# Optimization experiments

Measured on AMD Instinct MI355X. Metric: run time of the kernel, lower is better.

## Reference

```python
import jax, jax.numpy as jnp
import numpy as np

OBS_LEN = 8
N_PED = 2048      # total pedestrians
G = 64            # number of scenes (uniform size)
NP = N_PED // G   # pedestrians per scene = 32
H = 128           # action_decoder_hidden_dim == action_encoder_hidden_dim == f_in == f_out
DIN = 64          # action_encoder_input_dim
DD = 64           # distance_embedding_dim
NH = 4            # n_heads (hard-coded to 4 in GAT)


def setup_inputs() -> dict:
    key = jax.random.key(0)
    ks = jax.random.split(key, 16)
    s = 0.1  # weight scale (xavier-ish)
    starts = (jnp.arange(G) * NP).astype(jnp.int64)
    seq_start_end = jnp.stack([starts, starts + NP], axis=1)
    return {
        "obs_traj": jax.random.normal(ks[0], (OBS_LEN, N_PED, 2), jnp.float32),
        "goal_hidden_state": jax.random.normal(ks[1], (N_PED, H), jnp.float32),
        "goal": jax.random.normal(ks[2], (N_PED, 2), jnp.float32),
        "action": jax.random.normal(ks[3], (N_PED, 2), jnp.float32),
        "h0": jax.random.normal(ks[4], (N_PED, H), jnp.float32),
        "c0": jax.random.normal(ks[5], (N_PED, H), jnp.float32),
        "W_emb": jax.random.normal(ks[6], (2, DIN), jnp.float32) * s,
        "b_emb": jnp.zeros((DIN,), jnp.float32),
        "W_ih": jax.random.normal(ks[7], (4 * H, DIN), jnp.float32) * s,
        "W_hh": jax.random.normal(ks[8], (4 * H, H), jnp.float32) * s,
        "b_ih": jnp.zeros((4 * H,), jnp.float32),
        "b_hh": jnp.zeros((4 * H,), jnp.float32),
        "W_dist": jax.random.normal(ks[9], (8, DD), jnp.float32) * s,
        "b_dist": jnp.zeros((DD,), jnp.float32),
        "W_gate": jax.random.normal(ks[10], (DD, H), jnp.float32) * s,
        "b_gate": jnp.zeros((H,), jnp.float32),
        "gat_w": jax.random.normal(ks[11], (NH, 1, H, H), jnp.float32) * s,
        "gat_a": jax.random.normal(ks[12], (1, 1, 2 * H, 1), jnp.float32) * s,
        "gat_bias": jnp.zeros((H,), jnp.float32),
        "seq_start_end": seq_start_end,
    }


def _forward(obs_traj, goal_hidden_state, goal, action, h0, c0,
             W_emb, b_emb, W_ih, W_hh, b_ih, b_hh,
             W_dist, b_dist, W_gate, b_gate, gat_w, gat_a, gat_bias,
             seq_start_end):
    T, N, _ = obs_traj.shape
    g_num = seq_start_end.shape[0]
    n = N // g_num  # uniform group size

    # --- ActionEncoder: embed + LSTMCell loop over obs_len (lax.scan) ---
    x = jax.nn.relu(obs_traj.reshape(-1, 2) @ W_emb + b_emb).reshape(T, N, -1)

    def lstm_step(carry, xt):
        h, c = carry
        gates = xt @ W_ih.T + b_ih + h @ W_hh.T + b_hh  # torch gate order i,f,g,o
        i, f, g, o = jnp.split(gates, 4, axis=-1)
        c = jax.nn.sigmoid(f) * c + jax.nn.sigmoid(i) * jnp.tanh(g)
        h = jax.nn.sigmoid(o) * jnp.tanh(c)
        return (h, c), None

    (action_hidden, _), _ = jax.lax.scan(lstm_step, (h0, c0), x)  # [N, H]

    Hd = action_hidden.shape[-1]
    ahg = action_hidden.reshape(g_num, n, Hd)
    ghg = goal_hidden_state.reshape(g_num, n, Hd)
    glg = goal.reshape(g_num, n, 2)
    acg = action.reshape(g_num, n, 2)

    eye = jnp.eye(n, dtype=action_hidden.dtype)[:, :, None]  # [n, n, 1]

    def gat_group(ah, gh, gl, ac):
        # InteractionGate.cal_gate: dist[i,j] = [action_i, goal_i, action_j, goal_j]
        a_i = jnp.broadcast_to(ac[:, None, :], (n, n, 2))
        g_i = jnp.broadcast_to(gl[:, None, :], (n, n, 2))
        a_j = jnp.broadcast_to(ac[None, :, :], (n, n, 2))
        g_j = jnp.broadcast_to(gl[None, :, :], (n, n, 2))
        dist = jnp.concatenate([a_i, g_i, a_j, g_j], axis=-1)  # [n, n, 8]
        gate = jax.nn.sigmoid(jax.nn.relu(dist @ W_dist + b_dist) @ W_gate + b_gate)  # [n, n, H]

        # gate_action[i,j] = gate[i,j] * tanh(action_hidden[j])
        gate_action = gate * jnp.tanh(ah[None, :, :])
        # diagonal -> goal_hidden[i], off-diag -> gated action
        goal_action = eye * gh[None, :, :] + (1.0 - eye) * gate_action  # [n, n, H]

        h_other = jnp.concatenate([ah[:, None, :], goal_action], axis=1)  # [n, n+1, H]
        h_self = jnp.broadcast_to(ah[:, None, :], (n, n + 1, Hd))          # [n, n+1, H]

        # GraphAttentionLayer
        w = gat_w[:, 0]  # [NH, H, H]
        hs = jnp.einsum('nkf,hfo->hnko', h_self, w)   # [NH, n, n+1, H]
        ho = jnp.einsum('nkf,hfo->hnko', h_other, w)  # [NH, n, n+1, H]
        scores = jnp.concatenate([hs, ho], axis=-1) @ gat_a[0, 0, :, 0]  # [NH, n, n+1]
        alpha = jax.nn.softmax(jax.nn.leaky_relu(scores, 0.2), axis=-1)
        out = jnp.mean(jnp.sum(alpha[..., None] * ho, axis=2), axis=0)  # [n, H]
        return jax.nn.relu(out) + gat_bias

    out = jax.vmap(gat_group)(ahg, ghg, glg, acg)  # [G, n, H]
    return out.reshape(N, Hd)


def reference(obs_traj, goal_hidden_state, goal, action, h0, c0,
              W_emb, b_emb, W_ih, W_hh, b_ih, b_hh,
              W_dist, b_dist, W_gate, b_gate, gat_w, gat_a, gat_bias,
              seq_start_end):
    return _forward(obs_traj, goal_hidden_state, goal, action, h0, c0,
                    W_emb, b_emb, W_ih, W_hh, b_ih, b_hh,
                    W_dist, b_dist, W_gate, b_gate, gat_w, gat_a, gat_bias,
                    seq_start_end)
```

## Files before the change

kernel.cpp:

```cpp
#include <hip/hip_runtime.h>

#define N_PED 2048
#define NGROUP 64
#define NPG 32
#define HDIM 128
#define DIN 64
#define DDIM 64
#define NHEAD 4
#define TOBS 8

typedef __attribute__((ext_vector_type(8))) short bf16x8;
typedef __attribute__((ext_vector_type(4))) float f32x4;

__device__ __forceinline__ float sigm(float x){
    return __builtin_amdgcn_rcpf(1.f + __expf(-x));
}
__device__ __forceinline__ float tanh_fast(float x){
    return 1.f - 2.f*__builtin_amdgcn_rcpf(__expf(2.f*x) + 1.f);
}
__device__ __forceinline__ short f2bf(float f){
    unsigned u = __float_as_uint(f);
    unsigned r = (u + 0x7fffu + ((u >> 16) & 1u)) >> 16;
    return (short)r;
}
__device__ __forceinline__ float bf2f(unsigned short b){
    return __uint_as_float(((unsigned)b) << 16);
}
__device__ __forceinline__ unsigned pk2(float a, float b){
    return (unsigned)(unsigned short)f2bf(a) | ((unsigned)(unsigned short)f2bf(b) << 16);
}

#define WS_AHB   0
#define WS_TAHB  524288
#define WS_VW    1048576
#define WS_GF    1052672
#define WS_WF    1069056

__global__ __launch_bounds__(512) void prep_pack_kernel(
    const float* __restrict__ gat_w, const float* __restrict__ gat_a,
    const float* __restrict__ W_gate, unsigned char* __restrict__ ws)
{
    const int tid = threadIdx.x;
    if (blockIdx.x < 16) {
        __shared__ float sa[2*HDIM];
        __shared__ float red[32][8][2];
        float* VW = (float*)(ws + WS_VW);
        if (tid < 256) sa[tid] = gat_a[tid];
        __syncthreads();
        const int rl = (tid & 255) >> 3, ch = tid & 7;
        const int row = blockIdx.x*32 + rl;
        if (tid < 256) {
            const float* rp = gat_w + (size_t)row*HDIM + ch*16;
            float v = 0.f, w1 = 0.f;
            #pragma unroll
            for (int e = 0; e < 16; ++e) {
                float wv = rp[e];
                v  += wv * sa[HDIM + ch*16 + e];
                w1 += wv * sa[ch*16 + e];
            }
            red[rl][ch][0] = v; red[rl][ch][1] = w1;
        }
        __syncthreads();
        if (tid < 256 && ch == 0) {
            float sv = 0.f, sw = 0.f;
            #pragma unroll
            for (int e = 0; e < 8; ++e) { sv += red[rl][e][0]; sw += red[rl][e][1]; }
            VW[row]       = sv;
            VW[512 + row] = sw;
        }
    } else {
        const int id = (blockIdx.x - 16)*512 + tid;
        if (id >= 9216) return;
        uint4* Gf4 = reinterpret_cast<uint4*>(ws + WS_GF);
        uint4* Wf4 = reinterpret_cast<uint4*>(ws + WS_WF);
        if (id < 1024) {
            const int fid = id >> 6, L = id & 63;
            const int kt = fid >> 3, nt = fid & 7;
            const int q = L >> 4, ln = L & 15;
            float v[8];
            #pragma unroll
            for (int j = 0; j < 8; ++j)
                v[j] = W_gate[(size_t)(kt*32 + q*8 + j)*HDIM + nt*16 + ln];
            Gf4[id] = uint4{ pk2(v[0],v[1]), pk2(v[2],v[3]), pk2(v[4],v[5]), pk2(v[6],v[7]) };
        } else {
            const int id2 = id - 1024;
            const int fid = id2 >> 6, L = id2 & 63;
            const int kt = fid >> 3, nt = fid & 7;
            const int q = L >> 4, ln = L & 15;
            float v[8];
            #pragma unroll
            for (int j = 0; j < 8; ++j) {
                int F = kt*32 + q*8 + j;
                v[j] = gat_w[(size_t)(F >> 7)*16384 + (size_t)(F & 127)*HDIM + nt*16 + ln];
            }
            Wf4[id2] = uint4{ pk2(v[0],v[1]), pk2(v[2],v[3]), pk2(v[4],v[5]), pk2(v[6],v[7]) };
        }
    }
}

#define KPAD 216
__global__ __launch_bounds__(512, 1) void lstm_kernel(
    const float* __restrict__ obs, const float* __restrict__ h0,
    const float* __restrict__ c0,  const float* __restrict__ W_emb,
    const float* __restrict__ b_emb, const float* __restrict__ W_ih,
    const float* __restrict__ W_hh,  const float* __restrict__ b_ih,
    const float* __restrict__ b_hh,
    unsigned short* __restrict__ AHb, unsigned short* __restrict__ TAHb)
{
    __shared__ short Xl[2][16][KPAD];
    __shared__ float sEmb[192];

    const int tid  = threadIdx.x;
    const int ped0 = blockIdx.x * 8;
    const int w    = tid >> 6;
    const int lane = tid & 63;
    const int q    = lane >> 4;
    const int ln   = lane & 15;
    const int u    = w*16 + ln;

    if (tid < 192) sEmb[tid] = (tid < 128) ? W_emb[tid] : b_emb[tid - 128];

    bf16x8 bfr[4][6];
    #pragma unroll
    for (int idx = 0; idx < 4; ++idx) {
        const int n = idx*128 + u;
        #pragma unroll
        for (int kt = 0; kt < 6; ++kt) {
            const float* src = (kt < 2) ? (W_ih + (size_t)n*DIN  + kt*32 + q*8)
                                        : (W_hh + (size_t)n*HDIM + (kt-2)*32 + q*8);
            bf16x8 b;
            #pragma unroll
            for (int j = 0; j < 8; ++j) b[j] = f2bf(src[j]);
            bfr[idx][kt] = b;
        }
    }
    float bsv[4];
    #pragma unroll
    for (int idx = 0; idx < 4; ++idx) bsv[idx] = b_ih[idx*128 + u] + b_hh[idx*128 + u];

    float c_st[4];
    #pragma unroll
    for (int reg = 0; reg < 4; ++reg)
        c_st[reg] = c0[(size_t)(ped0 + ((q*4 + reg) & 7))*HDIM + u];

    #pragma unroll
    for (int reg = 0; reg < 4; ++reg)
        Xl[0][q*4 + reg][64 + u] = f2bf(h0[(size_t)(ped0 + ((q*4 + reg) & 7))*HDIM + u]);
    {
        const int pr = tid >> 5, d0 = (tid & 31)*2;
        const float2 ob = reinterpret_cast<const float2*>(obs)[(size_t)(ped0 + (pr & 7))];
        float x0 = fmaxf(ob.x*sEmb[d0]   + ob.y*sEmb[64+d0]   + sEmb[128+d0],   0.f);
        float x1 = fmaxf(ob.x*sEmb[d0+1] + ob.y*sEmb[64+d0+1] + sEmb[128+d0+1], 0.f);
        *reinterpret_cast<unsigned*>(&Xl[0][pr][d0]) = pk2(x0, x1);
    }
    __syncthreads();

    float hval[4];
    #pragma unroll
    for (int t = 0; t < TOBS; ++t) {
        const int cur = t & 1, nxt = cur ^ 1;

        if (t < TOBS-1) {
            const int pr = tid >> 5, d0 = (tid & 31)*2;
            const float2 ob = reinterpret_cast<const float2*>(obs)[(size_t)((t+1)*N_PED + ped0 + (pr & 7))];
            float x0 = fmaxf(ob.x*sEmb[d0]   + ob.y*sEmb[64+d0]   + sEmb[128+d0],   0.f);
            float x1 = fmaxf(ob.x*sEmb[d0+1] + ob.y*sEmb[64+d0+1] + sEmb[128+d0+1], 0.f);
            *reinterpret_cast<unsigned*>(&Xl[nxt][pr][d0]) = pk2(x0, x1);
        }

        bf16x8 afr[6];
        #pragma unroll
        for (int kt = 0; kt < 6; ++kt)
            afr[kt] = *reinterpret_cast<const bf16x8*>(&Xl[cur][ln][kt*32 + q*8]);

        f32x4 acc[4];
        #pragma unroll
        for (int idx = 0; idx < 4; ++idx) {
            f32x4 a = { bsv[idx], bsv[idx], bsv[idx], bsv[idx] };
            #pragma unroll
            for (int kt = 0; kt < 6; ++kt)
                a = __builtin_amdgcn_mfma_f32_16x16x32_bf16(afr[kt], bfr[idx][kt], a, 0, 0, 0);
            acc[idx] = a;
        }
        #pragma unroll
        for (int reg = 0; reg < 4; ++reg) {
            float c = sigm(acc[1][reg])*c_st[reg] + sigm(acc[0][reg])*tanh_fast(acc[2][reg]);
            c_st[reg] = c;
            hval[reg] = sigm(acc[3][reg])*tanh_fast(c);
        }

        if (t < TOBS-1) {
            #pragma unroll
            for (int reg = 0; reg < 4; ++reg)
                Xl[nxt][q*4 + reg][64 + u] = f2bf(hval[reg]);
            __syncthreads();
        }
    }

    if (q < 2) {
        #pragma unroll
        for (int reg = 0; reg < 4; ++reg) {
            const size_t off = (size_t)(ped0 + q*4 + reg)*HDIM + u;
            AHb[off]  = (unsigned short)f2bf(hval[reg]);
            TAHb[off] = (unsigned short)f2bf(tanh_fast(hval[reg]));
        }
    }
}

__global__ __launch_bounds__(256) void gat_kernel(
    const unsigned short* __restrict__ AHb,
    const unsigned short* __restrict__ TAHb,
    const float* __restrict__ VW,
    const unsigned char* __restrict__ ws,
    const float* __restrict__ ghs,
    const float* __restrict__ goal,
    const float* __restrict__ action,
    const float* __restrict__ W_dist,
    const float* __restrict__ b_dist,
    const float* __restrict__ b_gate,
    const float* __restrict__ gat_bias,
    float* __restrict__ out)
{
    __shared__ unsigned short sGAb[80][136];
    __shared__ unsigned short sTAHb[32][136];
    __shared__ unsigned short st1b[64][72];
    __shared__ unsigned short sU[4][520];
    __shared__ float sAl[2][4][34];
    __shared__ float sPj[80][8];
    __shared__ float sWd[8][64];
    __shared__ float sbd[64];
    __shared__ float sbg[128];
    __shared__ float sgb[128];
    __shared__ float sAC[32][2], sGL[32][2];

    const int tid = threadIdx.x;
    const int g   = blockIdx.x >> 3;
    const int i0  = (blockIdx.x & 7) * 4;
    const int p0  = g * NPG;
    const int w   = tid >> 6;
    const int L   = tid & 63;
    const int q   = L >> 4;
    const int ln  = L & 15;

    const bf16x8* Gf8 = reinterpret_cast<const bf16x8*>(ws + WS_GF);
    const bf16x8* Wf8 = reinterpret_cast<const bf16x8*>(ws + WS_WF);

    for (int s = tid; s < 512; s += 256) {
        int j = s >> 4, c = s & 15;
        *reinterpret_cast<uint4*>(&sTAHb[j][c*8]) =
            *reinterpret_cast<const uint4*>(&TAHb[(size_t)(p0 + j)*HDIM + c*8]);
    }
    if (tid < 128) {
        sbg[tid] = b_gate[tid];
        sgb[tid] = gat_bias[tid];
    } else if (tid < 192) {
        sbd[tid-128] = b_dist[tid-128];
    } else {
        int j = tid - 192;
        int pd = j & 31;
        if (j < 32) { const float2 a = reinterpret_cast<const float2*>(action)[p0+pd];
                      sAC[pd][0]=a.x; sAC[pd][1]=a.y; }
        else        { const float2 gl = reinterpret_cast<const float2*>(goal)[p0+pd];
                      sGL[pd][0]=gl.x; sGL[pd][1]=gl.y; }
    }
    if (tid < 256) {
        int rr = tid >> 6, k = tid & 63;
        sWd[rr][k]   = W_dist[rr*64 + k];
        sWd[rr+4][k] = W_dist[(rr+4)*64 + k];
    }

    bf16x8 vf[4];
    #pragma unroll
    for (int kt = 0; kt < 4; ++kt) {
        bf16x8 b;
        #pragma unroll
        for (int j = 0; j < 8; ++j) {
            int k = kt*32 + q*8 + j;
            float v = 0.f;
            if (ln < 4)      v = VW[ln*HDIM + k];
            else if (ln < 8) v = VW[512 + (ln-4)*HDIM + k];
            b[j] = f2bf(v);
        }
        vf[kt] = b;
    }
    __syncthreads();

    for (int half = 0; half < 2; ++half) {
        {
            const int k = tid & 63, mg = tid >> 6;
            float base[2];
            #pragma unroll
            for (int rh = 0; rh < 2; ++rh) {
                int i = i0 + half*2 + rh;
                base[rh] = sAC[i][0]*sWd[0][k] + sAC[i][1]*sWd[1][k]
                         + sGL[i][0]*sWd[2][k] + sGL[i][1]*sWd[3][k] + sbd[k];
            }
            #pragma unroll
            for (int mm = 0; mm < 16; ++mm) {
                int m = mg*16 + mm, j = m & 31;
                float v = base[m>>5] + sAC[j][0]*sWd[4][k] + sAC[j][1]*sWd[5][k]
                                     + sGL[j][0]*sWd[6][k] + sGL[j][1]*sWd[7][k];
                st1b[m][k] = (unsigned short)f2bf(fmaxf(v, 0.f));
            }
        }
        __syncthreads();

        {
            bf16x8 afr[2];
            #pragma unroll
            for (int kt = 0; kt < 2; ++kt)
                afr[kt] = *reinterpret_cast<const bf16x8*>(&st1b[w*16 + ln][kt*32 + q*8]);
            for (int nt = 0; nt < 8; ++nt) {
                float bg = sbg[nt*16 + ln];
                f32x4 a = { bg, bg, bg, bg };
                a = __builtin_amdgcn_mfma_f32_16x16x32_bf16(afr[0], Gf8[(0*8+nt)*64 + L], a, 0, 0, 0);
                a = __builtin_amdgcn_mfma_f32_16x16x32_bf16(afr[1], Gf8[(1*8+nt)*64 + L], a, 0, 0, 0);
                #pragma unroll
                for (int reg = 0; reg < 4; ++reg) {
                    int mrow = w*16 + q*4 + reg;
                    int n = nt*16 + ln;
                    float ga = sigm(a[reg]) * bf2f(sTAHb[mrow & 31][n]);
                    sGAb[mrow][n] = (unsigned short)f2bf(ga);
                }
            }
        }
        __syncthreads();

        {
            int rh = tid >> 7, f = tid & 127;
            int irow = i0 + half*2 + rh;
            sGAb[rh*32 + irow][f] = (unsigned short)f2bf(ghs[(size_t)(p0 + irow)*HDIM + f]);
            sGAb[64 + rh][f]      = AHb[(size_t)(p0 + irow)*HDIM + f];
        }
        __syncthreads();

        {
            int nmt = (w == 0) ? 2 : 1;
            for (int e = 0; e < nmt; ++e) {
                int mt = (e == 0) ? w : 4;
                bf16x8 afr;
                f32x4 a = { 0.f, 0.f, 0.f, 0.f };
                #pragma unroll
                for (int kt = 0; kt < 4; ++kt) {
                    afr = *reinterpret_cast<const bf16x8*>(&sGAb[mt*16 + ln][kt*32 + q*8]);
                    a = __builtin_amdgcn_mfma_f32_16x16x32_bf16(afr, vf[kt], a, 0, 0, 0);
                }
                if (ln < 8) {
                    #pragma unroll
                    for (int reg = 0; reg < 4; ++reg)
                        sPj[mt*16 + q*4 + reg][ln] = a[reg];
                }
            }
        }
        __syncthreads();

        if (tid < 8) {
            int rh = tid >> 2, h = tid & 3;
            float sa_ = sPj[64 + rh][4 + h];
            float x0  = sa_ + sPj[64 + rh][h];
            x0 = (x0 < 0.f) ? 0.2f*x0 : x0;
            float sum = 1.f;
            sAl[rh][h][0] = 1.f;
            for (int k = 1; k <= 32; ++k) {
                float x = sa_ + sPj[rh*32 + k - 1][h];
                x = (x < 0.f) ? 0.2f*x : x;
                float e = __expf(x - x0);
                sAl[rh][h][k] = e; sum += e;
            }
            float inv = 1.f/sum;
            for (int k = 0; k <= 32; ++k) sAl[rh][h][k] *= inv;
        }
        __syncthreads();

        {
            int rh = w & 1, ntb = (w >> 1) * 4;
            int r  = half*2 + rh;
            bf16x8 afr;
            #pragma unroll
            for (int jj = 0; jj < 8; ++jj)
                afr[jj] = f2bf(sAl[rh][ln & 3][1 + q*8 + jj]);
            for (int t = 0; t < 4; ++t) {
                int nt = ntb + t;
                bf16x8 bfr;
                #pragma unroll
                for (int jj = 0; jj < 8; ++jj)
                    bfr[jj] = (short)sGAb[rh*32 + q*8 + jj][nt*16 + ln];
                f32x4 a = { 0.f, 0.f, 0.f, 0.f };
                a = __builtin_amdgcn_mfma_f32_16x16x32_bf16(afr, bfr, a, 0, 0, 0);
                if (L < 16) {
                    #pragma unroll
                    for (int reg = 0; reg < 4; ++reg) {
                        float uv = a[reg] + sAl[rh][reg][0] * bf2f(sGAb[64 + rh][nt*16 + ln]);
                        sU[r][reg*HDIM + nt*16 + ln] = (unsigned short)f2bf(uv);
                    }
                }
            }
        }
        __syncthreads();
    }

    {
        bf16x8 afr[16];
        #pragma unroll
        for (int kt = 0; kt < 16; ++kt)
            afr[kt] = *reinterpret_cast<const bf16x8*>(&sU[ln & 3][kt*32 + q*8]);
        for (int e = 0; e < 2; ++e) {
            int nt = w*2 + e;
            f32x4 a = { 0.f, 0.f, 0.f, 0.f };
            #pragma unroll
            for (int kt = 0; kt < 16; ++kt)
                a = __builtin_amdgcn_mfma_f32_16x16x32_bf16(afr[kt], Wf8[(kt*8+nt)*64 + L], a, 0, 0, 0);
            if (L < 16) {
                int o = nt*16 + ln;
                #pragma unroll
                for (int reg = 0; reg < 4; ++reg) {
                    float val = fmaxf(a[reg]*0.25f, 0.f) + sgb[o];
                    out[(size_t)(p0 + i0 + reg)*HDIM + o] = val;
                }
            }
        }
    }
}

extern "C" void kernel_launch(void* const* d_in, const int* in_sizes, int n_in,
                              void* d_out, int out_size, void* d_ws, size_t ws_size,
                              hipStream_t stream) {
    const float* obs      = (const float*)d_in[0];
    const float* ghs      = (const float*)d_in[1];
    const float* goal     = (const float*)d_in[2];
    const float* action   = (const float*)d_in[3];
    const float* h0       = (const float*)d_in[4];
    const float* c0       = (const float*)d_in[5];
    const float* W_emb    = (const float*)d_in[6];
    const float* b_emb    = (const float*)d_in[7];
    const float* W_ih     = (const float*)d_in[8];
    const float* W_hh     = (const float*)d_in[9];
    const float* b_ih     = (const float*)d_in[10];
    const float* b_hh     = (const float*)d_in[11];
    const float* W_dist   = (const float*)d_in[12];
    const float* b_dist   = (const float*)d_in[13];
    const float* W_gate   = (const float*)d_in[14];
    const float* b_gate   = (const float*)d_in[15];
    const float* gat_w    = (const float*)d_in[16];
    const float* gat_a    = (const float*)d_in[17];
    const float* gat_bias = (const float*)d_in[18];

    unsigned char* ws = (unsigned char*)d_ws;
    unsigned short* AHb  = (unsigned short*)(ws + WS_AHB);
    unsigned short* TAHb = (unsigned short*)(ws + WS_TAHB);
    float* VW            = (float*)(ws + WS_VW);
    float* out = (float*)d_out;

    hipLaunchKernelGGL(prep_pack_kernel, dim3(34), dim3(512), 0, stream,
                       gat_w, gat_a, W_gate, ws);
    hipLaunchKernelGGL(lstm_kernel, dim3(256), dim3(512), 0, stream,
                       obs, h0, c0, W_emb, b_emb, W_ih, W_hh, b_ih, b_hh, AHb, TAHb);
    hipLaunchKernelGGL(gat_kernel,  dim3(512), dim3(256), 0, stream,
                       AHb, TAHb, VW, ws, ghs, goal, action,
                       W_dist, b_dist, b_gate, gat_bias, out);
}
```

Baseline: 142.7 us.

## Merge prep into LSTM launch and split GAT work across twice as many blocks

Folds the weight-packing prep kernel into the LSTM kernel as extra blocks, which removes one kernel launch and lets the prep run alongside the LSTM. The GAT kernel now handles two query rows per block instead of looping over two halves of four, doubling the grid to 1024 blocks for more parallelism. In exchange, the per-scene gate MLP and projection work is recomputed by twice as many blocks. It also drops the unroll on the LSTM time loop, relaxes its launch bounds, and splits the softmax sum into four accumulators with a fast reciprocal.

```diff
diff --git a/kernel.cpp b/kernel.cpp
--- a/kernel.cpp
+++ b/kernel.cpp
@@ -36,81 +36,83 @@
 #define WS_GF    1052672
 #define WS_WF    1069056
 
-__global__ __launch_bounds__(512) void prep_pack_kernel(
-    const float* __restrict__ gat_w, const float* __restrict__ gat_a,
-    const float* __restrict__ W_gate, unsigned char* __restrict__ ws)
-{
-    const int tid = threadIdx.x;
-    if (blockIdx.x < 16) {
-        __shared__ float sa[2*HDIM];
-        __shared__ float red[32][8][2];
-        float* VW = (float*)(ws + WS_VW);
-        if (tid < 256) sa[tid] = gat_a[tid];
-        __syncthreads();
-        const int rl = (tid & 255) >> 3, ch = tid & 7;
-        const int row = blockIdx.x*32 + rl;
-        if (tid < 256) {
-            const float* rp = gat_w + (size_t)row*HDIM + ch*16;
-            float v = 0.f, w1 = 0.f;
-            #pragma unroll
-            for (int e = 0; e < 16; ++e) {
-                float wv = rp[e];
-                v  += wv * sa[HDIM + ch*16 + e];
-                w1 += wv * sa[ch*16 + e];
-            }
-            red[rl][ch][0] = v; red[rl][ch][1] = w1;
-        }
-        __syncthreads();
-        if (tid < 256 && ch == 0) {
-            float sv = 0.f, sw = 0.f;
-            #pragma unroll
-            for (int e = 0; e < 8; ++e) { sv += red[rl][e][0]; sw += red[rl][e][1]; }
-            VW[row]       = sv;
-            VW[512 + row] = sw;
-        }
-    } else {
-        const int id = (blockIdx.x - 16)*512 + tid;
-        if (id >= 9216) return;
-        uint4* Gf4 = reinterpret_cast<uint4*>(ws + WS_GF);
-        uint4* Wf4 = reinterpret_cast<uint4*>(ws + WS_WF);
-        if (id < 1024) {
-            const int fid = id >> 6, L = id & 63;
-            const int kt = fid >> 3, nt = fid & 7;
-            const int q = L >> 4, ln = L & 15;
-            float v[8];
-            #pragma unroll
-            for (int j = 0; j < 8; ++j)
-                v[j] = W_gate[(size_t)(kt*32 + q*8 + j)*HDIM + nt*16 + ln];
-            Gf4[id] = uint4{ pk2(v[0],v[1]), pk2(v[2],v[3]), pk2(v[4],v[5]), pk2(v[6],v[7]) };
-        } else {
-            const int id2 = id - 1024;
-            const int fid = id2 >> 6, L = id2 & 63;
-            const int kt = fid >> 3, nt = fid & 7;
-            const int q = L >> 4, ln = L & 15;
-            float v[8];
-            #pragma unroll
-            for (int j = 0; j < 8; ++j) {
-                int F = kt*32 + q*8 + j;
-                v[j] = gat_w[(size_t)(F >> 7)*16384 + (size_t)(F & 127)*HDIM + nt*16 + ln];
-            }
-            Wf4[id2] = uint4{ pk2(v[0],v[1]), pk2(v[2],v[3]), pk2(v[4],v[5]), pk2(v[6],v[7]) };
-        }
-    }
-}
-
 #define KPAD 216
-__global__ __launch_bounds__(512, 1) void lstm_kernel(
+__global__ __launch_bounds__(512) void lstm_prep_kernel(
     const float* __restrict__ obs, const float* __restrict__ h0,
     const float* __restrict__ c0,  const float* __restrict__ W_emb,
     const float* __restrict__ b_emb, const float* __restrict__ W_ih,
     const float* __restrict__ W_hh,  const float* __restrict__ b_ih,
     const float* __restrict__ b_hh,
+    const float* __restrict__ gat_w, const float* __restrict__ gat_a,
+    const float* __restrict__ W_gate,
+    unsigned char* __restrict__ ws,
     unsigned short* __restrict__ AHb, unsigned short* __restrict__ TAHb)
 {
+    const int tid = threadIdx.x;
+
+    if (blockIdx.x >= 256) {
+        const int vb = blockIdx.x - 256;
+        if (vb < 16) {
+            __shared__ float sa[2*HDIM];
+            __shared__ float red[32][8][2];
+            float* VW = (float*)(ws + WS_VW);
+            if (tid < 256) sa[tid] = gat_a[tid];
+            __syncthreads();
+            const int rl = (tid & 255) >> 3, ch = tid & 7;
+            const int row = vb*32 + rl;
+            if (tid < 256) {
+                const float* rp = gat_w + (size_t)row*HDIM + ch*16;
+                float v = 0.f, w1 = 0.f;
+                #pragma unroll
+                for (int e = 0; e < 16; ++e) {
+                    float wv = rp[e];
+                    v  += wv * sa[HDIM + ch*16 + e];
+                    w1 += wv * sa[ch*16 + e];
+                }
+                red[rl][ch][0] = v; red[rl][ch][1] = w1;
+            }
+            __syncthreads();
+            if (tid < 256 && ch == 0) {
+                float sv = 0.f, sw = 0.f;
+                #pragma unroll
+                for (int e = 0; e < 8; ++e) { sv += red[rl][e][0]; sw += red[rl][e][1]; }
+                VW[row]       = sv;
+                VW[512 + row] = sw;
+            }
+        } else {
+            const int id = (vb - 16)*512 + tid;
+            if (id >= 9216) return;
+            uint4* Gf4 = reinterpret_cast<uint4*>(ws + WS_GF);
+            uint4* Wf4 = reinterpret_cast<uint4*>(ws + WS_WF);
+            if (id < 1024) {
+                const int fid = id >> 6, L = id & 63;
+                const int kt = fid >> 3, nt = fid & 7;
+                const int q = L >> 4, ln = L & 15;
+                float v[8];
+                #pragma unroll
+                for (int j = 0; j < 8; ++j)
+                    v[j] = W_gate[(size_t)(kt*32 + q*8 + j)*HDIM + nt*16 + ln];
+                Gf4[id] = uint4{ pk2(v[0],v[1]), pk2(v[2],v[3]), pk2(v[4],v[5]), pk2(v[6],v[7]) };
+            } else {
+                const int id2 = id - 1024;
+                const int fid = id2 >> 6, L = id2 & 63;
+                const int kt = fid >> 3, nt = fid & 7;
+                const int q = L >> 4, ln = L & 15;
+                float v[8];
+                #pragma unroll
+                for (int j = 0; j < 8; ++j) {
+                    int F = kt*32 + q*8 + j;
+                    v[j] = gat_w[(size_t)(F >> 7)*16384 + (size_t)(F & 127)*HDIM + nt*16 + ln];
+                }
+                Wf4[id2] = uint4{ pk2(v[0],v[1]), pk2(v[2],v[3]), pk2(v[4],v[5]), pk2(v[6],v[7]) };
+            }
+        }
+        return;
+    }
+
     __shared__ short Xl[2][16][KPAD];
     __shared__ float sEmb[192];
 
-    const int tid  = threadIdx.x;
     const int ped0 = blockIdx.x * 8;
     const int w    = tid >> 6;
     const int lane = tid & 63;
@@ -156,7 +158,6 @@
     __syncthreads();
 
     float hval[4];
-    #pragma unroll
     for (int t = 0; t < TOBS; ++t) {
         const int cur = t & 1, nxt = cur ^ 1;
 
@@ -224,7 +225,7 @@
     __shared__ unsigned short sGAb[80][136];
     __shared__ unsigned short sTAHb[32][136];
     __shared__ unsigned short st1b[64][72];
-    __shared__ unsigned short sU[4][520];
+    __shared__ unsigned short sU[2][520];
     __shared__ float sAl[2][4][34];
     __shared__ float sPj[80][8];
     __shared__ float sWd[8][64];
@@ -234,8 +235,8 @@
     __shared__ float sAC[32][2], sGL[32][2];
 
     const int tid = threadIdx.x;
-    const int g   = blockIdx.x >> 3;
-    const int i0  = (blockIdx.x & 7) * 4;
+    const int g   = blockIdx.x >> 4;
+    const int i0  = (blockIdx.x & 15) * 2;
     const int p0  = g * NPG;
     const int w   = tid >> 6;
     const int L   = tid & 63;
@@ -285,125 +286,130 @@
     }
     __syncthreads();
 
-    for (int half = 0; half < 2; ++half) {
-        {
-            const int k = tid & 63, mg = tid >> 6;
-            float base[2];
-            #pragma unroll
-            for (int rh = 0; rh < 2; ++rh) {
-                int i = i0 + half*2 + rh;
-                base[rh] = sAC[i][0]*sWd[0][k] + sAC[i][1]*sWd[1][k]
-                         + sGL[i][0]*sWd[2][k] + sGL[i][1]*sWd[3][k] + sbd[k];
-            }
-            #pragma unroll
-            for (int mm = 0; mm < 16; ++mm) {
-                int m = mg*16 + mm, j = m & 31;
-                float v = base[m>>5] + sAC[j][0]*sWd[4][k] + sAC[j][1]*sWd[5][k]
-                                     + sGL[j][0]*sWd[6][k] + sGL[j][1]*sWd[7][k];
-                st1b[m][k] = (unsigned short)f2bf(fmaxf(v, 0.f));
-            }
-        }
-        __syncthreads();
-
-        {
-            bf16x8 afr[2];
-            #pragma unroll
-            for (int kt = 0; kt < 2; ++kt)
-                afr[kt] = *reinterpret_cast<const bf16x8*>(&st1b[w*16 + ln][kt*32 + q*8]);
-            for (int nt = 0; nt < 8; ++nt) {
-                float bg = sbg[nt*16 + ln];
-                f32x4 a = { bg, bg, bg, bg };
-                a = __builtin_amdgcn_mfma_f32_16x16x32_bf16(afr[0], Gf8[(0*8+nt)*64 + L], a, 0, 0, 0);
-                a = __builtin_amdgcn_mfma_f32_16x16x32_bf16(afr[1], Gf8[(1*8+nt)*64 + L], a, 0, 0, 0);
+    {
+        const int k = tid & 63, mg = tid >> 6;
+        float base[2];
+        #pragma unroll
+        for (int rh = 0; rh < 2; ++rh) {
+            int i = i0 + rh;
+            base[rh] = sAC[i][0]*sWd[0][k] + sAC[i][1]*sWd[1][k]
+                     + sGL[i][0]*sWd[2][k] + sGL[i][1]*sWd[3][k] + sbd[k];
+        }
+        #pragma unroll
+        for (int mm = 0; mm < 16; ++mm) {
+            int m = mg*16 + mm, j = m & 31;
+            float v = base[m>>5] + sAC[j][0]*sWd[4][k] + sAC[j][1]*sWd[5][k]
+                                 + sGL[j][0]*sWd[6][k] + sGL[j][1]*sWd[7][k];
+            st1b[m][k] = (unsigned short)f2bf(fmaxf(v, 0.f));
+        }
+    }
+    __syncthreads();
+
+    {
+        bf16x8 afr[2];
+        #pragma unroll
+        for (int kt = 0; kt < 2; ++kt)
+            afr[kt] = *reinterpret_cast<const bf16x8*>(&st1b[w*16 + ln][kt*32 + q*8]);
+        for (int nt = 0; nt < 8; ++nt) {
+            float bg = sbg[nt*16 + ln];
+            f32x4 a = { bg, bg, bg, bg };
+            a = __builtin_amdgcn_mfma_f32_16x16x32_bf16(afr[0], Gf8[(0*8+nt)*64 + L], a, 0, 0, 0);
+            a = __builtin_amdgcn_mfma_f32_16x16x32_bf16(afr[1], Gf8[(1*8+nt)*64 + L], a, 0, 0, 0);
+            #pragma unroll
+            for (int reg = 0; reg < 4; ++reg) {
+                int mrow = w*16 + q*4 + reg;
+                int n = nt*16 + ln;
+                float ga = sigm(a[reg]) * bf2f(sTAHb[mrow & 31][n]);
+                sGAb[mrow][n] = (unsigned short)f2bf(ga);
+            }
+        }
+    }
+    __syncthreads();
+
+    {
+        int rh = tid >> 7, f = tid & 127;
+        int irow = i0 + rh;
+        sGAb[rh*32 + irow][f] = (unsigned short)f2bf(ghs[(size_t)(p0 + irow)*HDIM + f]);
+        sGAb[64 + rh][f]      = AHb[(size_t)(p0 + irow)*HDIM + f];
+    }
+    __syncthreads();
+
+    {
+        int nmt = (w == 0) ? 2 : 1;
+        for (int e = 0; e < nmt; ++e) {
+            int mt = (e == 0) ? w : 4;
+            bf16x8 afr;
+            f32x4 a = { 0.f, 0.f, 0.f, 0.f };
+            #pragma unroll
+            for (int kt = 0; kt < 4; ++kt) {
+                afr = *reinterpret_cast<const bf16x8*>(&sGAb[mt*16 + ln][kt*32 + q*8]);
+                a = __builtin_amdgcn_mfma_f32_16x16x32_bf16(afr, vf[kt], a, 0, 0, 0);
+            }
+            if (ln < 8) {
+                #pragma unroll
+                for (int reg = 0; reg < 4; ++reg)
+                    sPj[mt*16 + q*4 + reg][ln] = a[reg];
+            }
+        }
+    }
+    __syncthreads();
+
+    if (tid < 8) {
+        int rh = tid >> 2, h = tid & 3;
+        float sa_ = sPj[64 + rh][4 + h];
+        float x0  = sa_ + sPj[64 + rh][h];
+        x0 = (x0 < 0.f) ? 0.2f*x0 : x0;
+        sAl[rh][h][0] = 1.f;
+        float s0 = 1.f, s1 = 0.f, s2 = 0.f, s3 = 0.f;
+        #pragma unroll
+        for (int k = 1; k <= 32; k += 4) {
+            float xa = sa_ + sPj[rh*32 + k - 1][h];
+            float xb = sa_ + sPj[rh*32 + k    ][h];
+            float xc = sa_ + sPj[rh*32 + k + 1][h];
+            float xd = sa_ + sPj[rh*32 + k + 2][h];
+            xa = (xa < 0.f) ? 0.2f*xa : xa;  xb = (xb < 0.f) ? 0.2f*xb : xb;
+            xc = (xc < 0.f) ? 0.2f*xc : xc;  xd = (xd < 0.f) ? 0.2f*xd : xd;
+            float ea = __expf(xa - x0), eb = __expf(xb - x0);
+            float ec = __expf(xc - x0), ed = __expf(xd - x0);
+            sAl[rh][h][k]   = ea;  sAl[rh][h][k+1] = eb;
+            sAl[rh][h][k+2] = ec;  sAl[rh][h][k+3] = ed;
+            s0 += ea; s1 += eb; s2 += ec; s3 += ed;
+        }
+        float inv = __builtin_amdgcn_rcpf((s0 + s1) + (s2 + s3));
+        for (int k = 0; k <= 32; ++k) sAl[rh][h][k] *= inv;
+    }
+    __syncthreads();
+
+    {
+        int rh = w & 1, ntb = (w >> 1) * 4;
+        bf16x8 afr;
+        #pragma unroll
+        for (int jj = 0; jj < 8; ++jj)
+            afr[jj] = f2bf(sAl[rh][ln & 3][1 + q*8 + jj]);
+        for (int t = 0; t < 4; ++t) {
+            int nt = ntb + t;
+            bf16x8 bfr;
+            #pragma unroll
+            for (int jj = 0; jj < 8; ++jj)
+                bfr[jj] = (short)sGAb[rh*32 + q*8 + jj][nt*16 + ln];
+            f32x4 a = { 0.f, 0.f, 0.f, 0.f };
+            a = __builtin_amdgcn_mfma_f32_16x16x32_bf16(afr, bfr, a, 0, 0, 0);
+            if (L < 16) {
                 #pragma unroll
                 for (int reg = 0; reg < 4; ++reg) {
-                    int mrow = w*16 + q*4 + reg;
-                    int n = nt*16 + ln;
-                    float ga = sigm(a[reg]) * bf2f(sTAHb[mrow & 31][n]);
-                    sGAb[mrow][n] = (unsigned short)f2bf(ga);
+                    float uv = a[reg] + sAl[rh][reg][0] * bf2f(sGAb[64 + rh][nt*16 + ln]);
+                    sU[rh][reg*HDIM + nt*16 + ln] = (unsigned short)f2bf(uv);
                 }
             }
         }
-        __syncthreads();
-
-        {
-            int rh = tid >> 7, f = tid & 127;
-            int irow = i0 + half*2 + rh;
-            sGAb[rh*32 + irow][f] = (unsigned short)f2bf(ghs[(size_t)(p0 + irow)*HDIM + f]);
-            sGAb[64 + rh][f]      = AHb[(size_t)(p0 + irow)*HDIM + f];
-        }
-        __syncthreads();
-
-        {
-            int nmt = (w == 0) ? 2 : 1;
-            for (int e = 0; e < nmt; ++e) {
-                int mt = (e == 0) ? w : 4;
-                bf16x8 afr;
-                f32x4 a = { 0.f, 0.f, 0.f, 0.f };
-                #pragma unroll
-                for (int kt = 0; kt < 4; ++kt) {
-                    afr = *reinterpret_cast<const bf16x8*>(&sGAb[mt*16 + ln][kt*32 + q*8]);
-                    a = __builtin_amdgcn_mfma_f32_16x16x32_bf16(afr, vf[kt], a, 0, 0, 0);
-                }
-                if (ln < 8) {
-                    #pragma unroll
-                    for (int reg = 0; reg < 4; ++reg)
-                        sPj[mt*16 + q*4 + reg][ln] = a[reg];
-                }
-            }
-        }
-        __syncthreads();
-
-        if (tid < 8) {
-            int rh = tid >> 2, h = tid & 3;
-            float sa_ = sPj[64 + rh][4 + h];
-            float x0  = sa_ + sPj[64 + rh][h];
-            x0 = (x0 < 0.f) ? 0.2f*x0 : x0;
-            float sum = 1.f;
-            sAl[rh][h][0] = 1.f;
-            for (int k = 1; k <= 32; ++k) {
-                float x = sa_ + sPj[rh*32 + k - 1][h];
-                x = (x < 0.f) ? 0.2f*x : x;
-                float e = __expf(x - x0);
-                sAl[rh][h][k] = e; sum += e;
-            }
-            float inv = 1.f/sum;
-            for (int k = 0; k <= 32; ++k) sAl[rh][h][k] *= inv;
-        }
-        __syncthreads();
-
-        {
-            int rh = w & 1, ntb = (w >> 1) * 4;
-            int r  = half*2 + rh;
-            bf16x8 afr;
-            #pragma unroll
-            for (int jj = 0; jj < 8; ++jj)
-                afr[jj] = f2bf(sAl[rh][ln & 3][1 + q*8 + jj]);
-            for (int t = 0; t < 4; ++t) {
-                int nt = ntb + t;
-                bf16x8 bfr;
-                #pragma unroll
-                for (int jj = 0; jj < 8; ++jj)
-                    bfr[jj] = (short)sGAb[rh*32 + q*8 + jj][nt*16 + ln];
-                f32x4 a = { 0.f, 0.f, 0.f, 0.f };
-                a = __builtin_amdgcn_mfma_f32_16x16x32_bf16(afr, bfr, a, 0, 0, 0);
-                if (L < 16) {
-                    #pragma unroll
-                    for (int reg = 0; reg < 4; ++reg) {
-                        float uv = a[reg] + sAl[rh][reg][0] * bf2f(sGAb[64 + rh][nt*16 + ln]);
-                        sU[r][reg*HDIM + nt*16 + ln] = (unsigned short)f2bf(uv);
-                    }
-                }
-            }
-        }
-        __syncthreads();
-    }
+    }
+    __syncthreads();
 
     {
         bf16x8 afr[16];
         #pragma unroll
         for (int kt = 0; kt < 16; ++kt)
-            afr[kt] = *reinterpret_cast<const bf16x8*>(&sU[ln & 3][kt*32 + q*8]);
+            afr[kt] = *reinterpret_cast<const bf16x8*>(&sU[ln & 1][kt*32 + q*8]);
         for (int e = 0; e < 2; ++e) {
             int nt = w*2 + e;
             f32x4 a = { 0.f, 0.f, 0.f, 0.f };
@@ -413,7 +419,7 @@
             if (L < 16) {
                 int o = nt*16 + ln;
                 #pragma unroll
-                for (int reg = 0; reg < 4; ++reg) {
+                for (int reg = 0; reg < 2; ++reg) {
                     float val = fmaxf(a[reg]*0.25f, 0.f) + sgb[o];
                     out[(size_t)(p0 + i0 + reg)*HDIM + o] = val;
                 }
@@ -451,11 +457,10 @@
     float* VW            = (float*)(ws + WS_VW);
     float* out = (float*)d_out;
 
-    hipLaunchKernelGGL(prep_pack_kernel, dim3(34), dim3(512), 0, stream,
-                       gat_w, gat_a, W_gate, ws);
-    hipLaunchKernelGGL(lstm_kernel, dim3(256), dim3(512), 0, stream,
-                       obs, h0, c0, W_emb, b_emb, W_ih, W_hh, b_ih, b_hh, AHb, TAHb);
-    hipLaunchKernelGGL(gat_kernel,  dim3(512), dim3(256), 0, stream,
+    hipLaunchKernelGGL(lstm_prep_kernel, dim3(290), dim3(512), 0, stream,
+                       obs, h0, c0, W_emb, b_emb, W_ih, W_hh, b_ih, b_hh,
+                       gat_w, gat_a, W_gate, ws, AHb, TAHb);
+    hipLaunchKernelGGL(gat_kernel, dim3(1024), dim3(256), 0, stream,
                        AHb, TAHb, VW, ws, ghs, goal, action,
                        W_dist, b_dist, b_gate, gat_bias, out);
 }
```

New measurement: 139.5 us. 2.3% less time.
